# Performance work log

Hardware: AMD Instinct MI355X
Metric: run time of the kernel (lower is better)

Reference implementation:

```python
import jax, jax.numpy as jnp
import numpy as np

B, N, T, F, E = 64, 512, 50, 32, 32768  # batch, n_roi, n_timepoints, n_filters, n_edges


def setup_inputs() -> dict:
    key = jax.random.key(0)
    ks = jax.random.split(key, 24)
    s = 0.05
    inp = {
        "x": jax.random.normal(ks[0], (B, N, T), jnp.float32),
        "edge_index": jax.random.randint(ks[1], (2, E), 0, N, dtype=jnp.int64),
        "edge_weight": jax.random.uniform(ks[2], (E,), jnp.float32),
        # ChebConv K=2 weights: W[k] maps in->out for Chebyshev order k; shared bias.
        "conv1_W": jax.random.normal(ks[3], (2, T, F), jnp.float32) * s,
        "conv1_b": jnp.zeros((F,), jnp.float32),
        "conv2_W": jax.random.normal(ks[4], (2, F, F), jnp.float32) * s,
        "conv2_b": jnp.zeros((F,), jnp.float32),
        "conv3_W": jax.random.normal(ks[5], (2, F, F), jnp.float32) * s,
        "conv3_b": jnp.zeros((F,), jnp.float32),
        "conv4_W": jax.random.normal(ks[6], (2, F, F), jnp.float32) * s,
        "conv4_b": jnp.zeros((F,), jnp.float32),
        "conv5_W": jax.random.normal(ks[7], (2, F, F), jnp.float32) * s,
        "conv5_b": jnp.zeros((F,), jnp.float32),
        "conv6_W": jax.random.normal(ks[8], (2, F, F), jnp.float32) * s,
        "conv6_b": jnp.zeros((F,), jnp.float32),
        "fc1_W": jax.random.normal(ks[9], (F * N, 256), jnp.float32) * s,
        "fc1_b": jnp.zeros((256,), jnp.float32),
        "fc2_W": jax.random.normal(ks[10], (256, 128), jnp.float32) * s,
        "fc2_b": jnp.zeros((128,), jnp.float32),
        "fc3_W": jax.random.normal(ks[11], (128, 2), jnp.float32) * s,
        "fc3_b": jnp.zeros((2,), jnp.float32),
    }
    return inp


def reference(x, edge_index, edge_weight,
              conv1_W, conv1_b, conv2_W, conv2_b, conv3_W, conv3_b,
              conv4_W, conv4_b, conv5_W, conv5_b, conv6_W, conv6_b,
              fc1_W, fc1_b, fc2_W, fc2_b, fc3_W, fc3_b):
    n = x.shape[1]
    src, dst = edge_index[0], edge_index[1]
    # PyG ChebConv __norm__ (sym, lambda_max=2): remove self loops, build
    # L = I - D^-1/2 A D^-1/2, rescale 2L/lmax - I  ->  off-diag = -norm, diag = 0.
    w = jnp.where(src == dst, 0.0, edge_weight)
    deg = jax.ops.segment_sum(w, src, num_segments=n)
    dinv = jnp.where(deg > 0, jax.lax.rsqrt(deg), 0.0)
    norm = -(dinv[src] * w * dinv[dst])  # [E], static across all 6 layers

    def prop(hb):  # L_hat @ h for one sample: gather src, scatter-add to dst
        return jax.ops.segment_sum(norm[:, None] * hb[src], dst, num_segments=n)
    prop_b = jax.vmap(prop)

    def cheb(h, W, b):  # K=2: Tx0 = h, Tx1 = L_hat h
        return (jnp.einsum('bnc,cf->bnf', h, W[0])
                + jnp.einsum('bnc,cf->bnf', prop_b(h), W[1]) + b)

    h = jax.nn.relu(cheb(x, conv1_W, conv1_b))
    h = jax.nn.relu(cheb(h, conv2_W, conv2_b))
    h = jax.nn.relu(cheb(h, conv3_W, conv3_b))
    h = jax.nn.relu(cheb(h, conv4_W, conv4_b))
    h = jax.nn.relu(cheb(h, conv5_W, conv5_b))
    h = cheb(h, conv6_W, conv6_b)          # no relu after conv6 in original
    h = h.reshape(h.shape[0], -1)          # flatten node features per sample
    h = h @ fc1_W + fc1_b                  # dropout = identity at inference
    h = h @ fc2_W + fc2_b
    return h @ fc3_W + fc3_b
```

## Files before the change

kernel.cpp:

```cpp
#include <hip/hip_runtime.h>

#define NN 512
#define BB_ 64
#define EE 32768
#define TT 50
#define FF 32
#define NB 2048

#define OFF_LHAT 0
#define OFF_DEG  (512 * 512)
#define OFF_H    (OFF_DEG + 512)
#define OFF_G    (OFF_H + NN * NB)
#define OFF_F0   (OFF_G + NN * NB)
#define WS_FLOATS (OFF_F0 + NN * NB)


__global__ void k_zero_out(float* out, int n) {
    int i = blockIdx.x * blockDim.x + threadIdx.x;
    if (i < n) out[i] = 0.f;
}

__global__ void k_zero_range(float* p, int n) {
    int i = blockIdx.x * blockDim.x + threadIdx.x;
    if (i < n) p[i] = 0.f;
}

__global__ void k_deg(const int* __restrict__ ei, const float* __restrict__ ew,
                      float* __restrict__ deg) {
    int e = blockIdx.x * blockDim.x + threadIdx.x;
    if (e >= EE) return;
    int s = ei[e] & (NN - 1), d = ei[EE + e] & (NN - 1);
    if (s != d) atomicAdd(&deg[s], ew[e]);
}

__global__ void k_dinv(float* deg) {
    int i = threadIdx.x;
    float d = deg[i];
    deg[i] = (d > 0.f) ? rsqrtf(d) : 0.f;
}

__global__ void k_build(const int* __restrict__ ei, const float* __restrict__ ew,
                        const float* __restrict__ dinv, float* __restrict__ Lhat) {
    int e = blockIdx.x * blockDim.x + threadIdx.x;
    if (e >= EE) return;
    int s = ei[e] & (NN - 1), d = ei[EE + e] & (NN - 1);
    if (s == d) return;
    float nm = -(dinv[s] * ew[e] * dinv[d]);
    atomicAdd(&Lhat[d * NN + s], nm);
}

template<int CIN, bool FROM_X>
__global__ __launch_bounds__(256) void k_small(
        const float* __restrict__ Hin, const float* __restrict__ W,
        const float* __restrict__ bias,
        float* __restrict__ G, float* __restrict__ F0) {
    __shared__ float W0s[CIN * FF];
    __shared__ float W1s[CIN * FF];
    __shared__ float bs[FF];
    __shared__ float rows[64][CIN];
    const int tid = threadIdx.x;
    for (int i = tid; i < CIN * FF; i += 256) {
        W0s[i] = W[i];
        W1s[i] = W[CIN * FF + i];
    }
    if (tid < FF) bs[tid] = bias[tid];
    const int r0 = blockIdx.x * 64;
    for (int idx = tid; idx < 64 * CIN; idx += 256) {
        int r = idx / CIN, c = idx % CIN;
        int R = r0 + r;
        rows[r][c] = FROM_X ? Hin[((size_t)(R & 63) * NN + (R >> 6)) * CIN + c]
                            : Hin[(size_t)R * CIN + c];
    }
    __syncthreads();
    const int f = tid & 31, g = tid >> 5;
    float gacc[8] = {};
    float facc[8];
#pragma unroll
    for (int i = 0; i < 8; ++i) facc[i] = bs[f];
    for (int c = 0; c < CIN; ++c) {
        float w0 = W0s[c * FF + f], w1 = W1s[c * FF + f];
#pragma unroll
        for (int i = 0; i < 8; ++i) {
            float hv = rows[g + 8 * i][c];
            gacc[i] = fmaf(hv, w1, gacc[i]);
            facc[i] = fmaf(hv, w0, facc[i]);
        }
    }
#pragma unroll
    for (int i = 0; i < 8; ++i) {
        size_t o = (size_t)(r0 + g + 8 * i) * FF + f;
        G[o] = gacc[i];
        F0[o] = facc[i];
    }
}

template<bool RELU>
__global__ __launch_bounds__(256) void k_prop(
        const float* __restrict__ L, const float* __restrict__ G,
        const float* __restrict__ F0, float* __restrict__ H) {
    __shared__ float As[2][16][68];
    __shared__ float Bs[2][16][68];
    const int tid = threadIdx.x;
    const int tx = tid & 15, ty = tid >> 4;
    const int i0 = blockIdx.y * 64, j0 = blockIdx.x * 64;
    const int ar = tid >> 2, ac = (tid & 3) * 4;
    const int bk = tid >> 4, bj = (tid & 15) * 4;
    const float* Lp = L + (size_t)(i0 + ar) * NN + ac;
    const float* Gp = G + (size_t)bk * NB + j0 + bj;

    float acc[4][4] = {};
    float4 pa = *(const float4*)Lp;
    float4 pb = *(const float4*)Gp;

    for (int t = 0; t < 32; ++t) {
        const int buf = t & 1;
        As[buf][ac + 0][ar] = pa.x; As[buf][ac + 1][ar] = pa.y;
        As[buf][ac + 2][ar] = pa.z; As[buf][ac + 3][ar] = pa.w;
        *(float4*)&Bs[buf][bk][bj] = pb;
        __syncthreads();
        if (t < 31) {
            pa = *(const float4*)(Lp + (t + 1) * 16);
            pb = *(const float4*)(Gp + (size_t)(t + 1) * 16 * NB);
        }
#pragma unroll
        for (int k = 0; k < 16; ++k) {
            float a[4], b[4];
            *(float4*)a = *(const float4*)&As[buf][k][ty * 4];
            *(float4*)b = *(const float4*)&Bs[buf][k][tx * 4];
#pragma unroll
            for (int m = 0; m < 4; ++m) {
#pragma unroll
                for (int q = 0; q < 4; ++q)
                    acc[m][q] = fmaf(a[m], b[q], acc[m][q]);
            }
        }
    }

#pragma unroll
    for (int m = 0; m < 4; ++m) {
        const size_t o = (size_t)(i0 + ty * 4 + m) * NB + j0 + tx * 4;
        float4 f0 = *(const float4*)&F0[o];
        float4 v;
        v.x = acc[m][0] + f0.x; v.y = acc[m][1] + f0.y;
        v.z = acc[m][2] + f0.z; v.w = acc[m][3] + f0.w;
        if (RELU) {
            v.x = fmaxf(v.x, 0.f); v.y = fmaxf(v.y, 0.f);
            v.z = fmaxf(v.z, 0.f); v.w = fmaxf(v.w, 0.f);
        }
        *(float4*)&H[o] = v;
    }
}

__global__ __launch_bounds__(256) void k_fc1(const float* __restrict__ h,
                                             const float* __restrict__ W,
                                             float* __restrict__ P) {
    __shared__ float AT[128][68];
    const int tid = threadIdx.x;
    const int jg = blockIdx.x;
    const int kc = blockIdx.y;
    const float* hs = h + (size_t)kc * 4 * NB;
#pragma unroll
    for (int i = 0; i < 8; ++i) {
        int q = tid + i * 256;
        float4 v = *(const float4*)&hs[q * 4];
        int flat = q * 4;
        int nn = flat >> 11, rem = flat & 2047;
        int b = rem >> 5, f0 = rem & 31;
        int krow = nn * 32 + f0;
        AT[krow + 0][b] = v.x; AT[krow + 1][b] = v.y;
        AT[krow + 2][b] = v.z; AT[krow + 3][b] = v.w;
    }
    __syncthreads();
    const int tj = tid & 31, bq = tid >> 5;
    float acc[8] = {};
    const float* wp = W + (size_t)(kc * 128) * 256 + jg * 32 + tj;
#pragma unroll 8
    for (int k = 0; k < 128; ++k) {
        float w = wp[(size_t)k * 256];
        const float* ap = &AT[k][bq * 8];
        float4 a0 = *(const float4*)ap;
        float4 a1 = *(const float4*)(ap + 4);
        acc[0] = fmaf(a0.x, w, acc[0]); acc[1] = fmaf(a0.y, w, acc[1]);
        acc[2] = fmaf(a0.z, w, acc[2]); acc[3] = fmaf(a0.w, w, acc[3]);
        acc[4] = fmaf(a1.x, w, acc[4]); acc[5] = fmaf(a1.y, w, acc[5]);
        acc[6] = fmaf(a1.z, w, acc[6]); acc[7] = fmaf(a1.w, w, acc[7]);
    }
#pragma unroll
    for (int b2 = 0; b2 < 8; ++b2)
        P[(size_t)kc * 16384 + (bq * 8 + b2) * 256 + jg * 32 + tj] = acc[b2];
}

__global__ __launch_bounds__(128) void k_fc23(const float* __restrict__ P,
        const float* __restrict__ b1, const float* __restrict__ W2,
        const float* __restrict__ b2, const float* __restrict__ W3,
        const float* __restrict__ b3, float* __restrict__ out) {
    __shared__ float row[256];
    __shared__ float r2[128];
    const int m = blockIdx.x, j = threadIdx.x;
#pragma unroll
    for (int rep = 0; rep < 2; ++rep) {
        int k2 = j + rep * 128;
        float s = b1[k2];
#pragma unroll 8
        for (int kc = 0; kc < 128; ++kc)
            s += P[(size_t)kc * 16384 + m * 256 + k2];
        row[k2] = s;
    }
    __syncthreads();
    float acc = b2[j];
#pragma unroll 4
    for (int k = 0; k < 256; ++k)
        acc = fmaf(row[k], W2[k * 128 + j], acc);
    r2[j] = acc;
    __syncthreads();
    const int w = j >> 6, l = j & 63;
    float s2 = r2[l] * W3[l * 2 + w] + r2[l + 64] * W3[(l + 64) * 2 + w];
#pragma unroll
    for (int off = 32; off > 0; off >>= 1)
        s2 += __shfl_down(s2, off);
    if (l == 0) out[m * 2 + w] = s2 + b3[w];
}


extern "C" void kernel_launch(void* const* d_in, const int* in_sizes, int n_in,
                              void* d_out, int out_size, void* d_ws, size_t ws_size,
                              hipStream_t stream) {
    float* outp = (float*)d_out;
    if (ws_size < (size_t)WS_FLOATS * sizeof(float)) {
        k_zero_out<<<(out_size + 255) / 256, 256, 0, stream>>>(outp, out_size);
        return;
    }

    const float* x  = (const float*)d_in[0];
    const int*   ei = (const int*)d_in[1];
    const float* ew = (const float*)d_in[2];
    const float* cW[6] = {(const float*)d_in[3], (const float*)d_in[5],
                          (const float*)d_in[7], (const float*)d_in[9],
                          (const float*)d_in[11], (const float*)d_in[13]};
    const float* cb[6] = {(const float*)d_in[4], (const float*)d_in[6],
                          (const float*)d_in[8], (const float*)d_in[10],
                          (const float*)d_in[12], (const float*)d_in[14]};
    const float* fc1W = (const float*)d_in[15];
    const float* fc1b = (const float*)d_in[16];
    const float* fc2W = (const float*)d_in[17];
    const float* fc2b = (const float*)d_in[18];
    const float* fc3W = (const float*)d_in[19];
    const float* fc3b = (const float*)d_in[20];

    float* ws   = (float*)d_ws;
    float* Lhat = ws + OFF_LHAT;
    float* deg  = ws + OFF_DEG;
    float* H    = ws + OFF_H;
    float* G    = ws + OFF_G;
    float* F0   = ws + OFF_F0;
    float* P    = ws + OFF_G;

    k_zero_range<<<(OFF_DEG + 512 + 255) / 256, 256, 0, stream>>>(ws, OFF_DEG + 512);
    k_deg<<<EE / 256, 256, 0, stream>>>(ei, ew, deg);
    k_dinv<<<1, 512, 0, stream>>>(deg);
    k_build<<<EE / 256, 256, 0, stream>>>(ei, ew, deg, Lhat);

    dim3 pgrid(32, 8);
    k_small<TT, true ><<<512, 256, 0, stream>>>(x, cW[0], cb[0], G, F0);
    k_prop<true ><<<pgrid, 256, 0, stream>>>(Lhat, G, F0, H);
    k_small<FF, false><<<512, 256, 0, stream>>>(H, cW[1], cb[1], G, F0);
    k_prop<true ><<<pgrid, 256, 0, stream>>>(Lhat, G, F0, H);
    k_small<FF, false><<<512, 256, 0, stream>>>(H, cW[2], cb[2], G, F0);
    k_prop<true ><<<pgrid, 256, 0, stream>>>(Lhat, G, F0, H);
    k_small<FF, false><<<512, 256, 0, stream>>>(H, cW[3], cb[3], G, F0);
    k_prop<true ><<<pgrid, 256, 0, stream>>>(Lhat, G, F0, H);
    k_small<FF, false><<<512, 256, 0, stream>>>(H, cW[4], cb[4], G, F0);
    k_prop<true ><<<pgrid, 256, 0, stream>>>(Lhat, G, F0, H);
    k_small<FF, false><<<512, 256, 0, stream>>>(H, cW[5], cb[5], G, F0);
    k_prop<false><<<pgrid, 256, 0, stream>>>(Lhat, G, F0, H);

    dim3 fgrid(8, 128);
    k_fc1<<<fgrid, 256, 0, stream>>>(H, fc1W, P);
    k_fc23<<<64, 128, 0, stream>>>(P, fc1b, fc2W, fc2b, fc3W, fc3b, outp);
}
```

Measured before the change: 354.4 us.

## Run dense Laplacian propagation on MFMA using split-fp16 hi/lo products

Replaces the FP32 SIMT GEMM for L_hat @ G with MFMA f16 instructions. Each fp32 operand is split into a hi and lo half, and four products are accumulated to keep near-fp32 accuracy. The K dimension is split across two blocks (grid z=2), which write partial sums to separate buffers. The bias/ReLU epilogue and the merge of the two partials move into the next layer's k_small and into fc1. This adds a one-off L split kernel and extra partial-buffer traffic, and the extra traffic and the 4x MFMA count could eat the tensor-core gain.

```diff
diff --git a/kernel.cpp b/kernel.cpp
--- a/kernel.cpp
+++ b/kernel.cpp
@@ -7,12 +7,24 @@
 #define FF 32
 #define NB 2048
 
+typedef _Float16 f16x8 __attribute__((ext_vector_type(8)));
+typedef float    f32x4 __attribute__((ext_vector_type(4)));
+
 #define OFF_LHAT 0
-#define OFF_DEG  (512 * 512)
-#define OFF_H    (OFF_DEG + 512)
-#define OFF_G    (OFF_H + NN * NB)
-#define OFF_F0   (OFF_G + NN * NB)
+#define OFF_LP   (512 * 512)
+#define OFF_DEG  (OFF_LP + 512 * 512)
+#define OFF_HP0  (OFF_DEG + 512)
+#define OFF_HP1  (OFF_HP0 + NN * NB)
+#define OFF_GP   (OFF_HP1 + NN * NB)
+#define OFF_F0   (OFF_GP + NN * NB)
 #define WS_FLOATS (OFF_F0 + NN * NB)
+
+__device__ __forceinline__ unsigned pack_split(float v) {
+    _Float16 h = (_Float16)v;
+    _Float16 l = (_Float16)(v - (float)h);
+    return (unsigned)__builtin_bit_cast(unsigned short, h) |
+           ((unsigned)__builtin_bit_cast(unsigned short, l) << 16);
+}
 
 
 __global__ void k_zero_out(float* out, int n) {
@@ -49,11 +61,16 @@
     atomicAdd(&Lhat[d * NN + s], nm);
 }
 
-template<int CIN, bool FROM_X>
+__global__ void k_splitL(const float* __restrict__ L, unsigned* __restrict__ Lp) {
+    int i = blockIdx.x * 256 + threadIdx.x;
+    Lp[i] = pack_split(L[i]);
+}
+
+template<int CIN, int MODE>
 __global__ __launch_bounds__(256) void k_small(
-        const float* __restrict__ Hin, const float* __restrict__ W,
-        const float* __restrict__ bias,
-        float* __restrict__ G, float* __restrict__ F0) {
+        const float* __restrict__ A0, const float* __restrict__ A1,
+        const float* __restrict__ W, const float* __restrict__ bias,
+        unsigned* __restrict__ Gp, float* __restrict__ F0) {
     __shared__ float W0s[CIN * FF];
     __shared__ float W1s[CIN * FF];
     __shared__ float bs[FF];
@@ -68,8 +85,14 @@
     for (int idx = tid; idx < 64 * CIN; idx += 256) {
         int r = idx / CIN, c = idx % CIN;
         int R = r0 + r;
-        rows[r][c] = FROM_X ? Hin[((size_t)(R & 63) * NN + (R >> 6)) * CIN + c]
-                            : Hin[(size_t)R * CIN + c];
+        float v;
+        if (MODE == 0) {
+            v = A0[((size_t)(R & 63) * NN + (R >> 6)) * CIN + c];
+        } else {
+            size_t o = (size_t)R * CIN + c;
+            v = fmaxf(A0[o] + A1[o], 0.f);
+        }
+        rows[r][c] = v;
     }
     __syncthreads();
     const int f = tid & 31, g = tid >> 5;
@@ -89,80 +112,117 @@
 #pragma unroll
     for (int i = 0; i < 8; ++i) {
         size_t o = (size_t)(r0 + g + 8 * i) * FF + f;
-        G[o] = gacc[i];
+        Gp[o] = pack_split(gacc[i]);
         F0[o] = facc[i];
     }
 }
 
-template<bool RELU>
-__global__ __launch_bounds__(256) void k_prop(
-        const float* __restrict__ L, const float* __restrict__ G,
-        const float* __restrict__ F0, float* __restrict__ H) {
-    __shared__ float As[2][16][68];
-    __shared__ float Bs[2][16][68];
-    const int tid = threadIdx.x;
-    const int tx = tid & 15, ty = tid >> 4;
+__global__ __launch_bounds__(256) void k_prop_mfma(
+        const unsigned* __restrict__ Lp, const unsigned* __restrict__ Gp,
+        const float* __restrict__ F0,
+        float* __restrict__ Hp0, float* __restrict__ Hp1) {
+    __shared__ unsigned short Ahi[2][64][40], Alo[2][64][40];
+    __shared__ unsigned short Bhi[2][64][40], Blo[2][64][40];
+    const int tid  = threadIdx.x;
+    const int lane = tid & 63, w = tid >> 6;
+    const int wm = w >> 1, wn = w & 1;
+    const int grp = lane >> 4, l16 = lane & 15;
     const int i0 = blockIdx.y * 64, j0 = blockIdx.x * 64;
-    const int ar = tid >> 2, ac = (tid & 3) * 4;
-    const int bk = tid >> 4, bj = (tid & 15) * 4;
-    const float* Lp = L + (size_t)(i0 + ar) * NN + ac;
-    const float* Gp = G + (size_t)bk * NB + j0 + bj;
-
-    float acc[4][4] = {};
-    float4 pa = *(const float4*)Lp;
-    float4 pb = *(const float4*)Gp;
-
-    for (int t = 0; t < 32; ++t) {
+    const int kbase = blockIdx.z * 256;
+
+    const int arow = tid >> 5, ak = tid & 31;
+    const int brow = tid >> 6, bcol = tid & 63;
+
+    f32x4 acc[2][2] = {};
+    unsigned pa[8], pb[8];
+
+#pragma unroll
+    for (int i = 0; i < 8; ++i)
+        pa[i] = Lp[(size_t)(i0 + arow + i * 8) * NN + kbase + ak];
+#pragma unroll
+    for (int i = 0; i < 8; ++i)
+        pb[i] = Gp[(size_t)(kbase + brow + i * 4) * NB + j0 + bcol];
+
+    for (int t = 0; t < 8; ++t) {
         const int buf = t & 1;
-        As[buf][ac + 0][ar] = pa.x; As[buf][ac + 1][ar] = pa.y;
-        As[buf][ac + 2][ar] = pa.z; As[buf][ac + 3][ar] = pa.w;
-        *(float4*)&Bs[buf][bk][bj] = pb;
+#pragma unroll
+        for (int i = 0; i < 8; ++i) {
+            unsigned v = pa[i];
+            Ahi[buf][arow + i * 8][ak] = (unsigned short)v;
+            Alo[buf][arow + i * 8][ak] = (unsigned short)(v >> 16);
+        }
+#pragma unroll
+        for (int i = 0; i < 8; ++i) {
+            unsigned v = pb[i];
+            Bhi[buf][bcol][brow + i * 4] = (unsigned short)v;
+            Blo[buf][bcol][brow + i * 4] = (unsigned short)(v >> 16);
+        }
         __syncthreads();
-        if (t < 31) {
-            pa = *(const float4*)(Lp + (t + 1) * 16);
-            pb = *(const float4*)(Gp + (size_t)(t + 1) * 16 * NB);
-        }
-#pragma unroll
-        for (int k = 0; k < 16; ++k) {
-            float a[4], b[4];
-            *(float4*)a = *(const float4*)&As[buf][k][ty * 4];
-            *(float4*)b = *(const float4*)&Bs[buf][k][tx * 4];
-#pragma unroll
-            for (int m = 0; m < 4; ++m) {
-#pragma unroll
-                for (int q = 0; q < 4; ++q)
-                    acc[m][q] = fmaf(a[m], b[q], acc[m][q]);
+        if (t < 7) {
+            const int kc = kbase + (t + 1) * 32;
+#pragma unroll
+            for (int i = 0; i < 8; ++i)
+                pa[i] = Lp[(size_t)(i0 + arow + i * 8) * NN + kc + ak];
+#pragma unroll
+            for (int i = 0; i < 8; ++i)
+                pb[i] = Gp[(size_t)(kc + brow + i * 4) * NB + j0 + bcol];
+        }
+        f16x8 ah[2], al[2], bh[2], bl[2];
+#pragma unroll
+        for (int mi = 0; mi < 2; ++mi) {
+            ah[mi] = *(const f16x8*)&Ahi[buf][wm * 32 + mi * 16 + l16][grp * 8];
+            al[mi] = *(const f16x8*)&Alo[buf][wm * 32 + mi * 16 + l16][grp * 8];
+        }
+#pragma unroll
+        for (int ni = 0; ni < 2; ++ni) {
+            bh[ni] = *(const f16x8*)&Bhi[buf][wn * 32 + ni * 16 + l16][grp * 8];
+            bl[ni] = *(const f16x8*)&Blo[buf][wn * 32 + ni * 16 + l16][grp * 8];
+        }
+#pragma unroll
+        for (int mi = 0; mi < 2; ++mi)
+#pragma unroll
+            for (int ni = 0; ni < 2; ++ni) {
+                acc[mi][ni] = __builtin_amdgcn_mfma_f32_16x16x32_f16(al[mi], bl[ni], acc[mi][ni], 0, 0, 0);
+                acc[mi][ni] = __builtin_amdgcn_mfma_f32_16x16x32_f16(al[mi], bh[ni], acc[mi][ni], 0, 0, 0);
+                acc[mi][ni] = __builtin_amdgcn_mfma_f32_16x16x32_f16(ah[mi], bl[ni], acc[mi][ni], 0, 0, 0);
+                acc[mi][ni] = __builtin_amdgcn_mfma_f32_16x16x32_f16(ah[mi], bh[ni], acc[mi][ni], 0, 0, 0);
             }
-        }
-    }
-
-#pragma unroll
-    for (int m = 0; m < 4; ++m) {
-        const size_t o = (size_t)(i0 + ty * 4 + m) * NB + j0 + tx * 4;
-        float4 f0 = *(const float4*)&F0[o];
-        float4 v;
-        v.x = acc[m][0] + f0.x; v.y = acc[m][1] + f0.y;
-        v.z = acc[m][2] + f0.z; v.w = acc[m][3] + f0.w;
-        if (RELU) {
-            v.x = fmaxf(v.x, 0.f); v.y = fmaxf(v.y, 0.f);
-            v.z = fmaxf(v.z, 0.f); v.w = fmaxf(v.w, 0.f);
-        }
-        *(float4*)&H[o] = v;
-    }
-}
-
-__global__ __launch_bounds__(256) void k_fc1(const float* __restrict__ h,
+        __syncthreads();
+    }
+
+    float* Hp = blockIdx.z ? Hp1 : Hp0;
+#pragma unroll
+    for (int mi = 0; mi < 2; ++mi)
+#pragma unroll
+        for (int ni = 0; ni < 2; ++ni)
+#pragma unroll
+            for (int p = 0; p < 4; ++p) {
+                const int row = i0 + wm * 32 + mi * 16 + grp * 4 + p;
+                const int col = j0 + wn * 32 + ni * 16 + l16;
+                const size_t idx = (size_t)row * NB + col;
+                float v = acc[mi][ni][p];
+                if (blockIdx.z == 0) v += F0[idx];
+                Hp[idx] = v;
+            }
+}
+
+__global__ __launch_bounds__(256) void k_fc1(const float* __restrict__ h0,
+                                             const float* __restrict__ h1,
                                              const float* __restrict__ W,
                                              float* __restrict__ P) {
     __shared__ float AT[128][68];
     const int tid = threadIdx.x;
     const int jg = blockIdx.x;
     const int kc = blockIdx.y;
-    const float* hs = h + (size_t)kc * 4 * NB;
+    const size_t base = (size_t)kc * 4 * NB;
 #pragma unroll
     for (int i = 0; i < 8; ++i) {
         int q = tid + i * 256;
-        float4 v = *(const float4*)&hs[q * 4];
+        float4 v0 = *(const float4*)&h0[base + q * 4];
+        float4 v1 = *(const float4*)&h1[base + q * 4];
+        float4 v;
+        v.x = v0.x + v1.x; v.y = v0.y + v1.y;
+        v.z = v0.z + v1.z; v.w = v0.w + v1.w;
         int flat = q * 4;
         int nn = flat >> 11, rem = flat & 2047;
         int b = rem >> 5, f0 = rem & 31;
@@ -247,34 +307,37 @@
     const float* fc3W = (const float*)d_in[19];
     const float* fc3b = (const float*)d_in[20];
 
-    float* ws   = (float*)d_ws;
-    float* Lhat = ws + OFF_LHAT;
-    float* deg  = ws + OFF_DEG;
-    float* H    = ws + OFF_H;
-    float* G    = ws + OFF_G;
-    float* F0   = ws + OFF_F0;
-    float* P    = ws + OFF_G;
+    float*    ws   = (float*)d_ws;
+    float*    Lhat = ws + OFF_LHAT;
+    unsigned* Lp   = (unsigned*)(ws + OFF_LP);
+    float*    deg  = ws + OFF_DEG;
+    float*    Hp0  = ws + OFF_HP0;
+    float*    Hp1  = ws + OFF_HP1;
+    unsigned* Gp   = (unsigned*)(ws + OFF_GP);
+    float*    F0   = ws + OFF_F0;
+    float*    P    = ws + OFF_GP;
 
     k_zero_range<<<(OFF_DEG + 512 + 255) / 256, 256, 0, stream>>>(ws, OFF_DEG + 512);
     k_deg<<<EE / 256, 256, 0, stream>>>(ei, ew, deg);
     k_dinv<<<1, 512, 0, stream>>>(deg);
     k_build<<<EE / 256, 256, 0, stream>>>(ei, ew, deg, Lhat);
-
-    dim3 pgrid(32, 8);
-    k_small<TT, true ><<<512, 256, 0, stream>>>(x, cW[0], cb[0], G, F0);
-    k_prop<true ><<<pgrid, 256, 0, stream>>>(Lhat, G, F0, H);
-    k_small<FF, false><<<512, 256, 0, stream>>>(H, cW[1], cb[1], G, F0);
-    k_prop<true ><<<pgrid, 256, 0, stream>>>(Lhat, G, F0, H);
-    k_small<FF, false><<<512, 256, 0, stream>>>(H, cW[2], cb[2], G, F0);
-    k_prop<true ><<<pgrid, 256, 0, stream>>>(Lhat, G, F0, H);
-    k_small<FF, false><<<512, 256, 0, stream>>>(H, cW[3], cb[3], G, F0);
-    k_prop<true ><<<pgrid, 256, 0, stream>>>(Lhat, G, F0, H);
-    k_small<FF, false><<<512, 256, 0, stream>>>(H, cW[4], cb[4], G, F0);
-    k_prop<true ><<<pgrid, 256, 0, stream>>>(Lhat, G, F0, H);
-    k_small<FF, false><<<512, 256, 0, stream>>>(H, cW[5], cb[5], G, F0);
-    k_prop<false><<<pgrid, 256, 0, stream>>>(Lhat, G, F0, H);
+    k_splitL<<<NN * NN / 256, 256, 0, stream>>>(Lhat, Lp);
+
+    dim3 pgrid(32, 8, 2);
+    k_small<TT, 0><<<512, 256, 0, stream>>>(x, nullptr, cW[0], cb[0], Gp, F0);
+    k_prop_mfma<<<pgrid, 256, 0, stream>>>(Lp, Gp, F0, Hp0, Hp1);
+    k_small<FF, 1><<<512, 256, 0, stream>>>(Hp0, Hp1, cW[1], cb[1], Gp, F0);
+    k_prop_mfma<<<pgrid, 256, 0, stream>>>(Lp, Gp, F0, Hp0, Hp1);
+    k_small<FF, 1><<<512, 256, 0, stream>>>(Hp0, Hp1, cW[2], cb[2], Gp, F0);
+    k_prop_mfma<<<pgrid, 256, 0, stream>>>(Lp, Gp, F0, Hp0, Hp1);
+    k_small<FF, 1><<<512, 256, 0, stream>>>(Hp0, Hp1, cW[3], cb[3], Gp, F0);
+    k_prop_mfma<<<pgrid, 256, 0, stream>>>(Lp, Gp, F0, Hp0, Hp1);
+    k_small<FF, 1><<<512, 256, 0, stream>>>(Hp0, Hp1, cW[4], cb[4], Gp, F0);
+    k_prop_mfma<<<pgrid, 256, 0, stream>>>(Lp, Gp, F0, Hp0, Hp1);
+    k_small<FF, 1><<<512, 256, 0, stream>>>(Hp0, Hp1, cW[5], cb[5], Gp, F0);
+    k_prop_mfma<<<pgrid, 256, 0, stream>>>(Lp, Gp, F0, Hp0, Hp1);
 
     dim3 fgrid(8, 128);
-    k_fc1<<<fgrid, 256, 0, stream>>>(H, fc1W, P);
+    k_fc1<<<fgrid, 256, 0, stream>>>(Hp0, Hp1, fc1W, P);
     k_fc23<<<64, 128, 0, stream>>>(P, fc1b, fc2W, fc2b, fc3W, fc3b, outp);
 }
```

New measurement: 325.0 us. -8.3%, faster.

## Fuse Chebyshev layer into one MFMA kernel with split-fp16 precision and partial planes

Applied to the files above, without the earlier changes.

Replaces the per-layer pair of fp32 kernels (dense feature transform, then the L_hat GEMM) with a single fused kernel per layer. It runs on matrix cores with 16x16x32 f16 MFMA, splitting each fp32 operand into high and low fp16 halves so accuracy stays near fp32. Each block handles one sample, one 128-row output tile and one 128-column K slice of L_hat. It writes partial sums to four separate planes, which the next layer or fc1 sums while applying ReLU, so no atomics are needed. This removes the G/F0 intermediate round trips and replaces scalar FMAs with MFMAs. In exchange it adds a 4x larger output write and read per layer, four MFMAs per product, and recomputes L_hat·W1-style products redundantly across the tile blocks.

```diff
diff --git a/kernel.cpp b/kernel.cpp
--- a/kernel.cpp
+++ b/kernel.cpp
@@ -6,13 +6,29 @@
 #define TT 50
 #define FF 32
 #define NB 2048
+#define QN 128
+#define GSTR 136
+
+typedef _Float16 f16x8 __attribute__((ext_vector_type(8)));
+typedef float    f32x4 __attribute__((ext_vector_type(4)));
+typedef unsigned short u16t;
 
 #define OFF_LHAT 0
-#define OFF_DEG  (512 * 512)
-#define OFF_H    (OFF_DEG + 512)
-#define OFF_G    (OFF_H + NN * NB)
-#define OFF_F0   (OFF_G + NN * NB)
-#define WS_FLOATS (OFF_F0 + NN * NB)
+#define OFF_LHI  262144
+#define OFF_LLO  393216
+#define OFF_DEG  524288
+#define NPLANE   (NN * NB)
+#define OFF_HPA  524800
+#define OFF_HPB  (OFF_HPA + 4 * NPLANE)
+#define OFF_P    (OFF_HPB + 4 * NPLANE)
+#define WS_FLOATS (OFF_P + 128 * 16384)
+
+__device__ __forceinline__ void fsplit(float v, u16t& h, u16t& l) {
+    _Float16 hh = (_Float16)v;
+    _Float16 ll = (_Float16)(v - (float)hh);
+    h = __builtin_bit_cast(u16t, hh);
+    l = __builtin_bit_cast(u16t, ll);
+}
 
 
 __global__ void k_zero_out(float* out, int n) {
@@ -49,126 +65,191 @@
     atomicAdd(&Lhat[d * NN + s], nm);
 }
 
-template<int CIN, bool FROM_X>
-__global__ __launch_bounds__(256) void k_small(
-        const float* __restrict__ Hin, const float* __restrict__ W,
-        const float* __restrict__ bias,
-        float* __restrict__ G, float* __restrict__ F0) {
-    __shared__ float W0s[CIN * FF];
-    __shared__ float W1s[CIN * FF];
+__global__ void k_splitL(const float* __restrict__ L,
+                         u16t* __restrict__ Lhi, u16t* __restrict__ Llo) {
+    int i = blockIdx.x * 256 + threadIdx.x;
+    u16t h, l;
+    fsplit(L[i], h, l);
+    Lhi[i] = h; Llo[i] = l;
+}
+
+template<int CIN, int CINP, int MODE>
+__global__ __launch_bounds__(256) void k_layer(
+        const float* __restrict__ Xin, const float* __restrict__ Hin,
+        const u16t* __restrict__ Lhi, const u16t* __restrict__ Llo,
+        const float* __restrict__ W, const float* __restrict__ bias,
+        float* __restrict__ Hout) {
+    __shared__ u16t Hh[QN][CINP], Hl[QN][CINP];
+    __shared__ u16t Gh[FF][GSTR], Gl[FF][GSTR];
+    __shared__ u16t W1h[FF][CINP], W1l[FF][CINP];
     __shared__ float bs[FF];
-    __shared__ float rows[64][CIN];
-    const int tid = threadIdx.x;
-    for (int i = tid; i < CIN * FF; i += 256) {
-        W0s[i] = W[i];
-        W1s[i] = W[CIN * FF + i];
+    const int tid = threadIdx.x, bid = blockIdx.x;
+    const int b = bid >> 4, it = (bid >> 2) & 3, z = bid & 3;
+    const int lane = tid & 63, w = tid >> 6;
+    const int wm = w >> 1, wn = w & 1;
+    const int grp = lane >> 4, l16 = lane & 15;
+
+    if (MODE == 0) {
+        for (int idx = tid; idx < QN * CINP; idx += 256) {
+            int node = idx / CINP, c = idx % CINP;
+            float v = (c < CIN)
+                ? Xin[((size_t)b * NN + z * QN + node) * CIN + c] : 0.f;
+            fsplit(v, Hh[node][c], Hl[node][c]);
+        }
+    } else {
+        const float* p0 = Hin;
+        const float* p1 = Hin + NPLANE;
+        const float* p2 = Hin + 2 * NPLANE;
+        const float* p3 = Hin + 3 * NPLANE;
+#pragma unroll
+        for (int i = 0; i < 4; ++i) {
+            int q = tid + i * 256;
+            int node = q >> 3, c4 = (q & 7) * 4;
+            size_t o = (size_t)(z * QN + node) * NB + b * FF + c4;
+            float4 v0 = *(const float4*)&p0[o];
+            float4 v1 = *(const float4*)&p1[o];
+            float4 v2 = *(const float4*)&p2[o];
+            float4 v3 = *(const float4*)&p3[o];
+            float vv[4] = { fmaxf(v0.x + v1.x + v2.x + v3.x, 0.f),
+                            fmaxf(v0.y + v1.y + v2.y + v3.y, 0.f),
+                            fmaxf(v0.z + v1.z + v2.z + v3.z, 0.f),
+                            fmaxf(v0.w + v1.w + v2.w + v3.w, 0.f) };
+            ushort4 hh, ll;
+            fsplit(vv[0], hh.x, ll.x); fsplit(vv[1], hh.y, ll.y);
+            fsplit(vv[2], hh.z, ll.z); fsplit(vv[3], hh.w, ll.w);
+            *(ushort4*)&Hh[node][c4] = hh;
+            *(ushort4*)&Hl[node][c4] = ll;
+        }
+    }
+    for (int idx = tid; idx < FF * CINP; idx += 256) {
+        int f = idx & 31, c = idx >> 5;
+        float v = (c < CIN) ? W[(size_t)CIN * FF + c * FF + f] : 0.f;
+        fsplit(v, W1h[f][c], W1l[f][c]);
     }
     if (tid < FF) bs[tid] = bias[tid];
-    const int r0 = blockIdx.x * 64;
-    for (int idx = tid; idx < 64 * CIN; idx += 256) {
-        int r = idx / CIN, c = idx % CIN;
-        int R = r0 + r;
-        rows[r][c] = FROM_X ? Hin[((size_t)(R & 63) * NN + (R >> 6)) * CIN + c]
-                            : Hin[(size_t)R * CIN + c];
-    }
-    __syncthreads();
-    const int f = tid & 31, g = tid >> 5;
-    float gacc[8] = {};
-    float facc[8];
-#pragma unroll
-    for (int i = 0; i < 8; ++i) facc[i] = bs[f];
-    for (int c = 0; c < CIN; ++c) {
-        float w0 = W0s[c * FF + f], w1 = W1s[c * FF + f];
-#pragma unroll
-        for (int i = 0; i < 8; ++i) {
-            float hv = rows[g + 8 * i][c];
-            gacc[i] = fmaf(hv, w1, gacc[i]);
-            facc[i] = fmaf(hv, w0, facc[i]);
-        }
-    }
-#pragma unroll
-    for (int i = 0; i < 8; ++i) {
-        size_t o = (size_t)(r0 + g + 8 * i) * FF + f;
-        G[o] = gacc[i];
-        F0[o] = facc[i];
-    }
-}
-
-template<bool RELU>
-__global__ __launch_bounds__(256) void k_prop(
-        const float* __restrict__ L, const float* __restrict__ G,
-        const float* __restrict__ F0, float* __restrict__ H) {
-    __shared__ float As[2][16][68];
-    __shared__ float Bs[2][16][68];
-    const int tid = threadIdx.x;
-    const int tx = tid & 15, ty = tid >> 4;
-    const int i0 = blockIdx.y * 64, j0 = blockIdx.x * 64;
-    const int ar = tid >> 2, ac = (tid & 3) * 4;
-    const int bk = tid >> 4, bj = (tid & 15) * 4;
-    const float* Lp = L + (size_t)(i0 + ar) * NN + ac;
-    const float* Gp = G + (size_t)bk * NB + j0 + bj;
-
-    float acc[4][4] = {};
-    float4 pa = *(const float4*)Lp;
-    float4 pb = *(const float4*)Gp;
-
-    for (int t = 0; t < 32; ++t) {
-        const int buf = t & 1;
-        As[buf][ac + 0][ar] = pa.x; As[buf][ac + 1][ar] = pa.y;
-        As[buf][ac + 2][ar] = pa.z; As[buf][ac + 3][ar] = pa.w;
-        *(float4*)&Bs[buf][bk][bj] = pb;
-        __syncthreads();
-        if (t < 31) {
-            pa = *(const float4*)(Lp + (t + 1) * 16);
-            pb = *(const float4*)(Gp + (size_t)(t + 1) * 16 * NB);
-        }
-#pragma unroll
-        for (int k = 0; k < 16; ++k) {
-            float a[4], b[4];
-            *(float4*)a = *(const float4*)&As[buf][k][ty * 4];
-            *(float4*)b = *(const float4*)&Bs[buf][k][tx * 4];
-#pragma unroll
-            for (int m = 0; m < 4; ++m) {
-#pragma unroll
-                for (int q = 0; q < 4; ++q)
-                    acc[m][q] = fmaf(a[m], b[q], acc[m][q]);
+    __syncthreads();
+
+    f32x4 accg[2][2] = {};
+#pragma unroll
+    for (int kc = 0; kc < CINP / 32; ++kc) {
+        f16x8 gbh[2], gbl[2], gah[2], gal[2];
+#pragma unroll
+        for (int nt = 0; nt < 2; ++nt) {
+            gbh[nt] = *(const f16x8*)&W1h[nt * 16 + l16][kc * 32 + grp * 8];
+            gbl[nt] = *(const f16x8*)&W1l[nt * 16 + l16][kc * 32 + grp * 8];
+        }
+#pragma unroll
+        for (int mi = 0; mi < 2; ++mi) {
+            gah[mi] = *(const f16x8*)&Hh[w * 32 + mi * 16 + l16][kc * 32 + grp * 8];
+            gal[mi] = *(const f16x8*)&Hl[w * 32 + mi * 16 + l16][kc * 32 + grp * 8];
+        }
+#pragma unroll
+        for (int mi = 0; mi < 2; ++mi)
+#pragma unroll
+            for (int nt = 0; nt < 2; ++nt) {
+                accg[mi][nt] = __builtin_amdgcn_mfma_f32_16x16x32_f16(gal[mi], gbl[nt], accg[mi][nt], 0, 0, 0);
+                accg[mi][nt] = __builtin_amdgcn_mfma_f32_16x16x32_f16(gal[mi], gbh[nt], accg[mi][nt], 0, 0, 0);
+                accg[mi][nt] = __builtin_amdgcn_mfma_f32_16x16x32_f16(gah[mi], gbl[nt], accg[mi][nt], 0, 0, 0);
+                accg[mi][nt] = __builtin_amdgcn_mfma_f32_16x16x32_f16(gah[mi], gbh[nt], accg[mi][nt], 0, 0, 0);
             }
-        }
-    }
-
-#pragma unroll
-    for (int m = 0; m < 4; ++m) {
-        const size_t o = (size_t)(i0 + ty * 4 + m) * NB + j0 + tx * 4;
-        float4 f0 = *(const float4*)&F0[o];
-        float4 v;
-        v.x = acc[m][0] + f0.x; v.y = acc[m][1] + f0.y;
-        v.z = acc[m][2] + f0.z; v.w = acc[m][3] + f0.w;
-        if (RELU) {
-            v.x = fmaxf(v.x, 0.f); v.y = fmaxf(v.y, 0.f);
-            v.z = fmaxf(v.z, 0.f); v.w = fmaxf(v.w, 0.f);
-        }
-        *(float4*)&H[o] = v;
-    }
-}
-
-__global__ __launch_bounds__(256) void k_fc1(const float* __restrict__ h,
+    }
+#pragma unroll
+    for (int mi = 0; mi < 2; ++mi)
+#pragma unroll
+        for (int nt = 0; nt < 2; ++nt) {
+            ushort4 hh, ll;
+            fsplit(accg[mi][nt][0], hh.x, ll.x);
+            fsplit(accg[mi][nt][1], hh.y, ll.y);
+            fsplit(accg[mi][nt][2], hh.z, ll.z);
+            fsplit(accg[mi][nt][3], hh.w, ll.w);
+            int node = w * 32 + mi * 16 + grp * 4;
+            int f = nt * 16 + l16;
+            *(ushort4*)&Gh[f][node] = hh;
+            *(ushort4*)&Gl[f][node] = ll;
+        }
+    __syncthreads();
+
+    f32x4 acc[4] = {};
+    if (it == z) {
+#pragma unroll
+        for (int kc = 0; kc < CINP / 32; ++kc) {
+            f16x8 w0h, w0l;
+#pragma unroll
+            for (int j = 0; j < 8; ++j) {
+                int c = kc * 32 + grp * 8 + j;
+                float v = (c < CIN) ? W[(size_t)c * FF + wn * 16 + l16] : 0.f;
+                _Float16 hh = (_Float16)v;
+                w0h[j] = hh;
+                w0l[j] = (_Float16)(v - (float)hh);
+            }
+#pragma unroll
+            for (int mi = 0; mi < 4; ++mi) {
+                f16x8 ah = *(const f16x8*)&Hh[wm * 64 + mi * 16 + l16][kc * 32 + grp * 8];
+                f16x8 al = *(const f16x8*)&Hl[wm * 64 + mi * 16 + l16][kc * 32 + grp * 8];
+                acc[mi] = __builtin_amdgcn_mfma_f32_16x16x32_f16(al, w0l, acc[mi], 0, 0, 0);
+                acc[mi] = __builtin_amdgcn_mfma_f32_16x16x32_f16(al, w0h, acc[mi], 0, 0, 0);
+                acc[mi] = __builtin_amdgcn_mfma_f32_16x16x32_f16(ah, w0l, acc[mi], 0, 0, 0);
+                acc[mi] = __builtin_amdgcn_mfma_f32_16x16x32_f16(ah, w0h, acc[mi], 0, 0, 0);
+            }
+        }
+    }
+
+    const int i0 = it * QN;
+#pragma unroll
+    for (int kc = 0; kc < 4; ++kc) {
+        f16x8 bh = *(const f16x8*)&Gh[wn * 16 + l16][kc * 32 + grp * 8];
+        f16x8 bl = *(const f16x8*)&Gl[wn * 16 + l16][kc * 32 + grp * 8];
+#pragma unroll
+        for (int mi = 0; mi < 4; ++mi) {
+            size_t ao = (size_t)(i0 + wm * 64 + mi * 16 + l16) * NN
+                      + z * QN + kc * 32 + grp * 8;
+            f16x8 ah = *(const f16x8*)(Lhi + ao);
+            f16x8 al = *(const f16x8*)(Llo + ao);
+            acc[mi] = __builtin_amdgcn_mfma_f32_16x16x32_f16(al, bl, acc[mi], 0, 0, 0);
+            acc[mi] = __builtin_amdgcn_mfma_f32_16x16x32_f16(al, bh, acc[mi], 0, 0, 0);
+            acc[mi] = __builtin_amdgcn_mfma_f32_16x16x32_f16(ah, bl, acc[mi], 0, 0, 0);
+            acc[mi] = __builtin_amdgcn_mfma_f32_16x16x32_f16(ah, bh, acc[mi], 0, 0, 0);
+        }
+    }
+
+    float* Hp = Hout + (size_t)z * NPLANE;
+    const float bterm = (it == z) ? bs[wn * 16 + l16] : 0.f;
+#pragma unroll
+    for (int mi = 0; mi < 4; ++mi)
+#pragma unroll
+        for (int q = 0; q < 4; ++q) {
+            int row = i0 + wm * 64 + mi * 16 + grp * 4 + q;
+            Hp[(size_t)row * NB + b * FF + wn * 16 + l16] = acc[mi][q] + bterm;
+        }
+}
+
+__global__ __launch_bounds__(256) void k_fc1(const float* __restrict__ hp,
                                              const float* __restrict__ W,
                                              float* __restrict__ P) {
     __shared__ float AT[128][68];
     const int tid = threadIdx.x;
     const int jg = blockIdx.x;
     const int kc = blockIdx.y;
-    const float* hs = h + (size_t)kc * 4 * NB;
+    const size_t base = (size_t)kc * 4 * NB;
+    const float* p0 = hp;
+    const float* p1 = hp + NPLANE;
+    const float* p2 = hp + 2 * NPLANE;
+    const float* p3 = hp + 3 * NPLANE;
 #pragma unroll
     for (int i = 0; i < 8; ++i) {
         int q = tid + i * 256;
-        float4 v = *(const float4*)&hs[q * 4];
+        float4 v0 = *(const float4*)&p0[base + q * 4];
+        float4 v1 = *(const float4*)&p1[base + q * 4];
+        float4 v2 = *(const float4*)&p2[base + q * 4];
+        float4 v3 = *(const float4*)&p3[base + q * 4];
         int flat = q * 4;
-        int nn = flat >> 11, rem = flat & 2047;
+        int nn2 = flat >> 11, rem = flat & 2047;
         int b = rem >> 5, f0 = rem & 31;
-        int krow = nn * 32 + f0;
-        AT[krow + 0][b] = v.x; AT[krow + 1][b] = v.y;
-        AT[krow + 2][b] = v.z; AT[krow + 3][b] = v.w;
+        int krow = nn2 * 32 + f0;
+        AT[krow + 0][b] = v0.x + v1.x + v2.x + v3.x;
+        AT[krow + 1][b] = v0.y + v1.y + v2.y + v3.y;
+        AT[krow + 2][b] = v0.z + v1.z + v2.z + v3.z;
+        AT[krow + 3][b] = v0.w + v1.w + v2.w + v3.w;
     }
     __syncthreads();
     const int tj = tid & 31, bq = tid >> 5;
@@ -176,14 +257,14 @@
     const float* wp = W + (size_t)(kc * 128) * 256 + jg * 32 + tj;
 #pragma unroll 8
     for (int k = 0; k < 128; ++k) {
-        float w = wp[(size_t)k * 256];
+        float wv = wp[(size_t)k * 256];
         const float* ap = &AT[k][bq * 8];
         float4 a0 = *(const float4*)ap;
         float4 a1 = *(const float4*)(ap + 4);
-        acc[0] = fmaf(a0.x, w, acc[0]); acc[1] = fmaf(a0.y, w, acc[1]);
-        acc[2] = fmaf(a0.z, w, acc[2]); acc[3] = fmaf(a0.w, w, acc[3]);
-        acc[4] = fmaf(a1.x, w, acc[4]); acc[5] = fmaf(a1.y, w, acc[5]);
-        acc[6] = fmaf(a1.z, w, acc[6]); acc[7] = fmaf(a1.w, w, acc[7]);
+        acc[0] = fmaf(a0.x, wv, acc[0]); acc[1] = fmaf(a0.y, wv, acc[1]);
+        acc[2] = fmaf(a0.z, wv, acc[2]); acc[3] = fmaf(a0.w, wv, acc[3]);
+        acc[4] = fmaf(a1.x, wv, acc[4]); acc[5] = fmaf(a1.y, wv, acc[5]);
+        acc[6] = fmaf(a1.z, wv, acc[6]); acc[7] = fmaf(a1.w, wv, acc[7]);
     }
 #pragma unroll
     for (int b2 = 0; b2 < 8; ++b2)
@@ -249,32 +330,27 @@
 
     float* ws   = (float*)d_ws;
     float* Lhat = ws + OFF_LHAT;
+    u16t*  Lhi  = (u16t*)(ws + OFF_LHI);
+    u16t*  Llo  = (u16t*)(ws + OFF_LLO);
     float* deg  = ws + OFF_DEG;
-    float* H    = ws + OFF_H;
-    float* G    = ws + OFF_G;
-    float* F0   = ws + OFF_F0;
-    float* P    = ws + OFF_G;
+    float* HA   = ws + OFF_HPA;
+    float* HB   = ws + OFF_HPB;
+    float* P    = ws + OFF_P;
 
     k_zero_range<<<(OFF_DEG + 512 + 255) / 256, 256, 0, stream>>>(ws, OFF_DEG + 512);
     k_deg<<<EE / 256, 256, 0, stream>>>(ei, ew, deg);
     k_dinv<<<1, 512, 0, stream>>>(deg);
     k_build<<<EE / 256, 256, 0, stream>>>(ei, ew, deg, Lhat);
-
-    dim3 pgrid(32, 8);
-    k_small<TT, true ><<<512, 256, 0, stream>>>(x, cW[0], cb[0], G, F0);
-    k_prop<true ><<<pgrid, 256, 0, stream>>>(Lhat, G, F0, H);
-    k_small<FF, false><<<512, 256, 0, stream>>>(H, cW[1], cb[1], G, F0);
-    k_prop<true ><<<pgrid, 256, 0, stream>>>(Lhat, G, F0, H);
-    k_small<FF, false><<<512, 256, 0, stream>>>(H, cW[2], cb[2], G, F0);
-    k_prop<true ><<<pgrid, 256, 0, stream>>>(Lhat, G, F0, H);
-    k_small<FF, false><<<512, 256, 0, stream>>>(H, cW[3], cb[3], G, F0);
-    k_prop<true ><<<pgrid, 256, 0, stream>>>(Lhat, G, F0, H);
-    k_small<FF, false><<<512, 256, 0, stream>>>(H, cW[4], cb[4], G, F0);
-    k_prop<true ><<<pgrid, 256, 0, stream>>>(Lhat, G, F0, H);
-    k_small<FF, false><<<512, 256, 0, stream>>>(H, cW[5], cb[5], G, F0);
-    k_prop<false><<<pgrid, 256, 0, stream>>>(Lhat, G, F0, H);
+    k_splitL<<<NN * NN / 256, 256, 0, stream>>>(Lhat, Lhi, Llo);
+
+    k_layer<TT, 64, 0><<<1024, 256, 0, stream>>>(x,  nullptr, Lhi, Llo, cW[0], cb[0], HA);
+    k_layer<FF, 32, 1><<<1024, 256, 0, stream>>>(nullptr, HA, Lhi, Llo, cW[1], cb[1], HB);
+    k_layer<FF, 32, 1><<<1024, 256, 0, stream>>>(nullptr, HB, Lhi, Llo, cW[2], cb[2], HA);
+    k_layer<FF, 32, 1><<<1024, 256, 0, stream>>>(nullptr, HA, Lhi, Llo, cW[3], cb[3], HB);
+    k_layer<FF, 32, 1><<<1024, 256, 0, stream>>>(nullptr, HB, Lhi, Llo, cW[4], cb[4], HA);
+    k_layer<FF, 32, 1><<<1024, 256, 0, stream>>>(nullptr, HA, Lhi, Llo, cW[5], cb[5], HB);
 
     dim3 fgrid(8, 128);
-    k_fc1<<<fgrid, 256, 0, stream>>>(H, fc1W, P);
+    k_fc1<<<fgrid, 256, 0, stream>>>(HB, fc1W, P);
     k_fc23<<<64, 128, 0, stream>>>(P, fc1b, fc2W, fc2b, fc3W, fc3b, outp);
 }
```

Result: no change. 358.4 us (+1.1%).
